# Kernel tuning notes

Measured on AMD Instinct MI355X. Metric: run time of the kernel, lower is better.

The kernel has to match this reference:

```python
import jax, jax.numpy as jnp
import numpy as np

B, S, H, DH = 2, 2048, 16, 64
DIM = H * DH          # 1024
WIN = 512             # relpos_win_size
LN_EPS = 1e-5


def setup_inputs() -> dict:
    key = jax.random.key(0)
    ks = jax.random.split(key, 8)
    return {
        "q": jax.random.normal(ks[0], (B, S, H, DH), dtype=jnp.float32),
        "k": jax.random.normal(ks[1], (B, S, H, DH), dtype=jnp.float32),
        "relpos_emb": jax.random.normal(ks[2], (WIN, DIM), dtype=jnp.float32),
        "ln_scale": jnp.ones((DIM,), dtype=jnp.float32),
        "ln_bias": jnp.zeros((DIM,), dtype=jnp.float32),
        "Wq": jax.random.normal(ks[3], (DIM, DIM), dtype=jnp.float32),
        "bq": jnp.zeros((DIM,), dtype=jnp.float32),
        "Wk": jax.random.normal(ks[4], (DIM, DIM), dtype=jnp.float32),
        "bk": jnp.zeros((DIM,), dtype=jnp.float32),
    }


def reference(q, k, relpos_emb, ln_scale, ln_bias, Wq, bq, Wk, bk):
    b, nq, h, dh = q.shape
    nk = k.shape[1]
    win = relpos_emb.shape[0]

    # LayerNorm over the embedding dim (use_pos_layer_norm=True); dropout is identity (eval).
    mu = jnp.mean(relpos_emb, axis=-1, keepdims=True)
    var = jnp.mean(jnp.square(relpos_emb - mu), axis=-1, keepdims=True)
    pe = (relpos_emb - mu) * jax.lax.rsqrt(var + LN_EPS) * ln_scale + ln_bias

    qpos = jnp.arange(nq)
    kpos = jnp.arange(nk)
    rel = jnp.clip(kpos[None, :] - qpos[:, None], -(win - 1), 0) + (win - 1)
    idx = jnp.broadcast_to(rel[None, None, :, :], (b, h, nq, nk))

    # Linear projections of the (small) relpos table, split into heads.
    relpos_k = (pe @ Wk.T + bk).reshape(win, h, dh)  # relpos_k_proj
    relpos_q = (pe @ Wq.T + bq).reshape(win, h, dh)  # relpos_q_proj

    # query-to-position: scores over window then gather along window axis (dim 3).
    query_pos_scores = jnp.einsum('bnhx,khx->bhnk', q, relpos_k)
    logits_query_pos = jnp.take_along_axis(query_pos_scores, idx, axis=3)  # [b,h,nq,nk]

    key_pos_scores = jnp.einsum('bnhx,khx->bhkn', k, relpos_q)
    logits_pos_key = jnp.take_along_axis(key_pos_scores, idx, axis=2)      # [b,h,nq,nk]

    # scale_factor = 1 + True + True = 3 (static constant, omitted from array outputs)
    return logits_pos_key, logits_query_pos, relpos_q, relpos_k
```

## Files before the change

### kernel.cpp

```cpp
#include <hip/hip_runtime.h>

#define BB 2
#define S 2048
#define H 16
#define DH 64
#define DIM 1024
#define WIN 512

#define OUT_PK 0
#define OUT_QP 134217728
#define OUT_RQ 268435456
#define OUT_RK 268959744

#define WS_C0Q   1024
#define WS_C511Q (1024 + 65536)
#define WS_C0K   (1024 + 2*65536)
#define WS_C511K (1024 + 3*65536)
#define WS_BF_BASE 263168

typedef short bf16x8 __attribute__((ext_vector_type(8)));
typedef float f32x4 __attribute__((ext_vector_type(4)));

__device__ inline short f2bf(float f) {
    union { float f; unsigned int u; } cv; cv.f = f;
    unsigned int u = cv.u + 0x7FFFu + ((cv.u >> 16) & 1u);
    return (short)(u >> 16);
}

__device__ inline float bf2f(short s) {
    union { unsigned int u; float f; } cv;
    cv.u = ((unsigned int)(unsigned short)s) << 16;
    return cv.f;
}

__global__ __launch_bounds__(256) void prep1(const float* __restrict__ emb,
        const float* __restrict__ lnsc, const float* __restrict__ lnbi,
        const float* __restrict__ Wq, const float* __restrict__ bq,
        const float* __restrict__ Wk, const float* __restrict__ bk,
        const float* __restrict__ q, const float* __restrict__ k,
        float* __restrict__ out, short* __restrict__ rqbf, short* __restrict__ rkbf,
        short* __restrict__ qbf, short* __restrict__ kbf) {
    __shared__ short As[64 * 72];
    __shared__ short Bs[64 * 72];
    __shared__ float smu[64];
    __shared__ float srs[64];
    int bid = blockIdx.x;
    int t = threadIdx.x;

    if (bid >= 256) {
        int cb = bid - 256;
        int z = cb >> 10;
        int blk = cb & 1023;
        const float* src = z ? k : q;
        short* dst = z ? kbf : qbf;
        int e0 = (blk * 256 + t) * 16;
        int c = e0 & 63, hh = (e0 >> 6) & 15, n = (e0 >> 10) & 2047, b = e0 >> 21;
        short* dbase = dst + (((size_t)(b * 16 + hh) * 2048) + n) * 64 + c;
#pragma unroll
        for (int i = 0; i < 4; ++i) {
            float4 v = *reinterpret_cast<const float4*>(src + e0 + i * 4);
            short4 o = { f2bf(v.x), f2bf(v.y), f2bf(v.z), f2bf(v.w) };
            *reinterpret_cast<short4*>(dbase + i * 4) = o;
        }
        return;
    }

    const float* W    = (bid >> 7) ? Wk : Wq;
    const float* bias = (bid >> 7) ? bk : bq;
    float* o = out + ((bid >> 7) ? OUT_RK : OUT_RQ);
    short* bfo = (bid >> 7) ? rkbf : rqbf;
    int r0 = (bid & 7) * 64;
    int d0 = ((bid >> 3) & 15) * 64;

    {
        int rr = t >> 2, p = t & 3;
        const float4* rp = reinterpret_cast<const float4*>(emb + (r0 + rr) * DIM + p * 256);
        float s = 0.f, sq = 0.f;
#pragma unroll
        for (int i = 0; i < 64; ++i) {
            float4 v = rp[i];
            s  += v.x + v.y + v.z + v.w;
            sq += v.x * v.x + v.y * v.y + v.z * v.z + v.w * v.w;
        }
        s += __shfl_xor(s, 1); sq += __shfl_xor(sq, 1);
        s += __shfl_xor(s, 2); sq += __shfl_xor(sq, 2);
        if (p == 0) {
            float mu = s / DIM;
            float var = sq / DIM - mu * mu;
            smu[rr] = mu;
            srs[rr] = rsqrtf(var + 1e-5f);
        }
    }
    __syncthreads();

    int lane = t & 63, w = t >> 6, lr = lane & 15, lg = lane >> 4;
    int srow = t >> 2, seg = (t & 3) * 16;
    float mu = smu[srow], rs = srs[srow];

    f32x4 acc[4] = {};
    for (int c0 = 0; c0 < DIM; c0 += 64) {
        const float4* ep = reinterpret_cast<const float4*>(emb + (size_t)(r0 + srow) * DIM + c0 + seg);
        const float4* wp = reinterpret_cast<const float4*>(W + (size_t)(d0 + srow) * DIM + c0 + seg);
        short4* ad = reinterpret_cast<short4*>(&As[srow * 72 + seg]);
        short4* wd = reinterpret_cast<short4*>(&Bs[srow * 72 + seg]);
#pragma unroll
        for (int i = 0; i < 4; ++i) {
            float4 v = ep[i], wv = wp[i];
            int cb2 = c0 + seg + i * 4;
            float4 sc = *reinterpret_cast<const float4*>(lnsc + cb2);
            float4 bi = *reinterpret_cast<const float4*>(lnbi + cb2);
            short4 a4 = { f2bf((v.x - mu) * rs * sc.x + bi.x),
                          f2bf((v.y - mu) * rs * sc.y + bi.y),
                          f2bf((v.z - mu) * rs * sc.z + bi.z),
                          f2bf((v.w - mu) * rs * sc.w + bi.w) };
            short4 w4 = { f2bf(wv.x), f2bf(wv.y), f2bf(wv.z), f2bf(wv.w) };
            ad[i] = a4;
            wd[i] = w4;
        }
        __syncthreads();
#pragma unroll
        for (int kk = 0; kk < 2; ++kk) {
            bf16x8 a = *reinterpret_cast<const bf16x8*>(&As[(w * 16 + lr) * 72 + kk * 32 + lg * 8]);
#pragma unroll
            for (int cg = 0; cg < 4; ++cg) {
                bf16x8 b = *reinterpret_cast<const bf16x8*>(&Bs[(cg * 16 + lr) * 72 + kk * 32 + lg * 8]);
                acc[cg] = __builtin_amdgcn_mfma_f32_16x16x32_bf16(a, b, acc[cg], 0, 0, 0);
            }
        }
        __syncthreads();
    }
#pragma unroll
    for (int cg = 0; cg < 4; ++cg) {
        int col = d0 + cg * 16 + lr;
        float bv = bias[col];
        int hh = col >> 6, cc = col & 63;
#pragma unroll
        for (int reg = 0; reg < 4; ++reg) {
            int rr = r0 + w * 16 + lg * 4 + reg;
            float val = acc[cg][reg] + bv;
            o[(size_t)rr * DIM + col] = val;
            bfo[((size_t)(hh * 512) + rr) * 64 + cc] = f2bf(val);
        }
    }
}

__global__ __launch_bounds__(256) void cvec(const short* __restrict__ qbf,
        const short* __restrict__ kbf, const short* __restrict__ rqbf,
        const short* __restrict__ rkbf, float* __restrict__ ws) {
    int cid = blockIdx.x;
    int z = cid >> 10;
    int rem = cid & 1023;
    int bh = rem >> 5, rb = rem & 31;
    int t = threadIdx.x;
    int rr = t >> 2, p = t & 3;
    int n = rb * 64 + rr;
    int h = bh & 15;
    const short* X = (z ? kbf : qbf) + ((size_t)bh * 2048 + n) * 64 + p * 16;
    const short* T = (z ? rqbf : rkbf) + (size_t)h * 512 * 64 + p * 16;
    bf16x8 x0 = *reinterpret_cast<const bf16x8*>(X);
    bf16x8 x1 = *reinterpret_cast<const bf16x8*>(X + 8);
    bf16x8 a0 = *reinterpret_cast<const bf16x8*>(T);
    bf16x8 a1 = *reinterpret_cast<const bf16x8*>(T + 8);
    bf16x8 c0 = *reinterpret_cast<const bf16x8*>(T + 511 * 64);
    bf16x8 c1 = *reinterpret_cast<const bf16x8*>(T + 511 * 64 + 8);
    float d0 = 0.f, d1 = 0.f;
#pragma unroll
    for (int e = 0; e < 8; ++e) {
        float xa = bf2f(x0[e]), xb = bf2f(x1[e]);
        d0 += xa * bf2f(a0[e]) + xb * bf2f(a1[e]);
        d1 += xa * bf2f(c0[e]) + xb * bf2f(c1[e]);
    }
    d0 += __shfl_xor(d0, 1); d0 += __shfl_xor(d0, 2);
    d1 += __shfl_xor(d1, 1); d1 += __shfl_xor(d1, 2);
    if (p == 0) {
        int o = bh * S + n;
        if (!z) { ws[WS_C0Q + o] = d0; ws[WS_C511Q + o] = d1; }
        else    { ws[WS_C0K + o] = d0; ws[WS_C511K + o] = d1; }
    }
}

__global__ __launch_bounds__(256) void outk(const short* __restrict__ qbf,
        const short* __restrict__ kbf, const short* __restrict__ rqbf,
        const short* __restrict__ rkbf, const float* __restrict__ ws,
        float* __restrict__ out) {
    __shared__ short Yt[64 * 132];

    int bid = blockIdx.x;
    int wg = (bid & 7) * 8192 + (bid >> 3);
    int PK = wg >> 15;
    int bh = (wg >> 10) & 31; int h = bh & 15;
    int nt = (wg >> 5) & 31, jt = wg & 31;
    int n0 = nt * 64, j0 = jt * 64;
    int jlo = nt > 8 ? nt - 8 : 0;
    int t = threadIdx.x;
    float* obase = out + (PK ? OUT_PK : OUT_QP) + (size_t)bh * S * S;

    if (jt < jlo || jt > nt) {
        int left = jt < jlo;
        const float* cv = ws + (PK ? (left ? WS_C0K : WS_C511K)
                                   : (left ? WS_C0Q : WS_C511Q)) + bh * S;
        int col4 = t & 15, r0w = t >> 4;
        if (PK) {
            f32x4 v = *reinterpret_cast<const f32x4*>(cv + j0 + col4 * 4);
#pragma unroll
            for (int i = 0; i < 4; ++i) {
                int n = n0 + r0w + i * 16;
                __builtin_nontemporal_store(v,
                    reinterpret_cast<f32x4*>(obase + (size_t)n * S + j0 + col4 * 4));
            }
        } else {
#pragma unroll
            for (int i = 0; i < 4; ++i) {
                int n = n0 + r0w + i * 16;
                float vs = cv[n];
                f32x4 v = { vs, vs, vs, vs };
                __builtin_nontemporal_store(v,
                    reinterpret_cast<f32x4*>(obase + (size_t)n * S + j0 + col4 * 4));
            }
        }
        return;
    }

    int rlo = 511 + j0 - (n0 + 63); rlo = rlo < 0 ? 0 : rlo;

    const short* xb = (PK ? kbf : qbf) + ((size_t)bh * 2048 + (PK ? j0 : n0)) * 64;
    const short* tbase = (PK ? rqbf : rkbf) + (size_t)h * 512 * 64;

    int lane = t & 63, w = t >> 6, lr = lane & 15, lg = lane >> 4;
    const short* arow = xb + (w * 16 + lr) * 64 + lg * 8;
    bf16x8 a0 = *reinterpret_cast<const bf16x8*>(arow);
    bf16x8 a1 = *reinterpret_cast<const bf16x8*>(arow + 32);

    bf16x8 b0s[8], b1s[8];
#pragma unroll
    for (int s = 0; s < 8; ++s) {
        int trow = rlo + s * 16 + lr;
        trow = trow > 511 ? 511 : trow;
        const short* brow = tbase + trow * 64 + lg * 8;
        b0s[s] = *reinterpret_cast<const bf16x8*>(brow);
        b1s[s] = *reinterpret_cast<const bf16x8*>(brow + 32);
    }
#pragma unroll
    for (int s = 0; s < 8; ++s) {
        f32x4 acc = {0.f, 0.f, 0.f, 0.f};
        acc = __builtin_amdgcn_mfma_f32_16x16x32_bf16(a0, b0s[s], acc, 0, 0, 0);
        acc = __builtin_amdgcn_mfma_f32_16x16x32_bf16(a1, b1s[s], acc, 0, 0, 0);
#pragma unroll
        for (int reg = 0; reg < 4; ++reg)
            Yt[(w * 16 + lg * 4 + reg) * 132 + s * 16 + lr] = f2bf(acc[reg]);
    }
    __syncthreads();

    int tx = t & 15, ty = t >> 4;
#pragma unroll
    for (int i = 0; i < 4; ++i) {
        int rowi = ty + i * 16;
        int n = n0 + rowi;
        float vv[4];
#pragma unroll
        for (int jj = 0; jj < 4; ++jj) {
            int j = j0 + tx * 4 + jj;
            int rel = 511 + j - n;
            rel = rel < 0 ? 0 : (rel > 511 ? 511 : rel);
            int g = rel - rlo;
            int m = PK ? (tx * 4 + jj) : rowi;
            vv[jj] = bf2f(Yt[m * 132 + g]);
        }
        f32x4 v = { vv[0], vv[1], vv[2], vv[3] };
        __builtin_nontemporal_store(v,
            reinterpret_cast<f32x4*>(obase + (size_t)n * S + j0 + tx * 4));
    }
}

extern "C" void kernel_launch(void* const* d_in, const int* in_sizes, int n_in,
                              void* d_out, int out_size, void* d_ws, size_t ws_size,
                              hipStream_t stream) {
    const float* q    = (const float*)d_in[0];
    const float* k    = (const float*)d_in[1];
    const float* emb  = (const float*)d_in[2];
    const float* lnsc = (const float*)d_in[3];
    const float* lnbi = (const float*)d_in[4];
    const float* Wq   = (const float*)d_in[5];
    const float* bq   = (const float*)d_in[6];
    const float* Wk   = (const float*)d_in[7];
    const float* bk   = (const float*)d_in[8];
    float* out = (float*)d_out;
    float* ws  = (float*)d_ws;

    short* qbf  = (short*)(ws + WS_BF_BASE);
    short* kbf  = qbf + (size_t)4194304;
    short* rqbf = kbf + (size_t)4194304;
    short* rkbf = rqbf + (size_t)524288;

    prep1<<<dim3(2304), dim3(256), 0, stream>>>(emb, lnsc, lnbi, Wq, bq, Wk, bk,
                                                q, k, out, rqbf, rkbf, qbf, kbf);
    cvec<<<dim3(2048), dim3(256), 0, stream>>>(qbf, kbf, rqbf, rkbf, ws);
    outk<<<dim3(65536), dim3(256), 0, stream>>>(qbf, kbf, rqbf, rkbf, ws, out);
}
```

Before: 233.4 us.

## Fuse clamp-vector computation into output kernel and merge flat tiles into wide panels

```diff
diff --git a/kernel.cpp b/kernel.cpp
--- a/kernel.cpp
+++ b/kernel.cpp
@@ -12,10 +12,6 @@
 #define OUT_RQ 268435456
 #define OUT_RK 268959744
 
-#define WS_C0Q   1024
-#define WS_C511Q (1024 + 65536)
-#define WS_C0K   (1024 + 2*65536)
-#define WS_C511K (1024 + 3*65536)
 #define WS_BF_BASE 263168
 
 typedef short bf16x8 __attribute__((ext_vector_type(8)));
@@ -31,6 +27,18 @@
     union { unsigned int u; float f; } cv;
     cv.u = ((unsigned int)(unsigned short)s) << 16;
     return cv.f;
+}
+
+__device__ inline float dot64(const short* __restrict__ x, const short* __restrict__ y) {
+    float d = 0.f;
+#pragma unroll
+    for (int c = 0; c < 8; ++c) {
+        bf16x8 a = *reinterpret_cast<const bf16x8*>(x + c * 8);
+        bf16x8 b = *reinterpret_cast<const bf16x8*>(y + c * 8);
+#pragma unroll
+        for (int e = 0; e < 8; ++e) d += bf2f(a[e]) * bf2f(b[e]);
+    }
+    return d;
 }
 
 __global__ __launch_bounds__(256) void prep1(const float* __restrict__ emb,
@@ -144,83 +152,92 @@
     }
 }
 
-__global__ __launch_bounds__(256) void cvec(const short* __restrict__ qbf,
-        const short* __restrict__ kbf, const short* __restrict__ rqbf,
-        const short* __restrict__ rkbf, float* __restrict__ ws) {
-    int cid = blockIdx.x;
-    int z = cid >> 10;
-    int rem = cid & 1023;
-    int bh = rem >> 5, rb = rem & 31;
-    int t = threadIdx.x;
-    int rr = t >> 2, p = t & 3;
-    int n = rb * 64 + rr;
-    int h = bh & 15;
-    const short* X = (z ? kbf : qbf) + ((size_t)bh * 2048 + n) * 64 + p * 16;
-    const short* T = (z ? rqbf : rkbf) + (size_t)h * 512 * 64 + p * 16;
-    bf16x8 x0 = *reinterpret_cast<const bf16x8*>(X);
-    bf16x8 x1 = *reinterpret_cast<const bf16x8*>(X + 8);
-    bf16x8 a0 = *reinterpret_cast<const bf16x8*>(T);
-    bf16x8 a1 = *reinterpret_cast<const bf16x8*>(T + 8);
-    bf16x8 c0 = *reinterpret_cast<const bf16x8*>(T + 511 * 64);
-    bf16x8 c1 = *reinterpret_cast<const bf16x8*>(T + 511 * 64 + 8);
-    float d0 = 0.f, d1 = 0.f;
-#pragma unroll
-    for (int e = 0; e < 8; ++e) {
-        float xa = bf2f(x0[e]), xb = bf2f(x1[e]);
-        d0 += xa * bf2f(a0[e]) + xb * bf2f(a1[e]);
-        d1 += xa * bf2f(c0[e]) + xb * bf2f(c1[e]);
-    }
-    d0 += __shfl_xor(d0, 1); d0 += __shfl_xor(d0, 2);
-    d1 += __shfl_xor(d1, 1); d1 += __shfl_xor(d1, 2);
-    if (p == 0) {
-        int o = bh * S + n;
-        if (!z) { ws[WS_C0Q + o] = d0; ws[WS_C511Q + o] = d1; }
-        else    { ws[WS_C0K + o] = d0; ws[WS_C511K + o] = d1; }
-    }
-}
-
 __global__ __launch_bounds__(256) void outk(const short* __restrict__ qbf,
         const short* __restrict__ kbf, const short* __restrict__ rqbf,
-        const short* __restrict__ rkbf, const float* __restrict__ ws,
-        float* __restrict__ out) {
+        const short* __restrict__ rkbf, float* __restrict__ out) {
     __shared__ short Yt[64 * 132];
+    float* c_sm = reinterpret_cast<float*>(Yt);
 
     int bid = blockIdx.x;
-    int wg = (bid & 7) * 8192 + (bid >> 3);
-    int PK = wg >> 15;
-    int bh = (wg >> 10) & 31; int h = bh & 15;
-    int nt = (wg >> 5) & 31, jt = wg & 31;
-    int n0 = nt * 64, j0 = jt * 64;
-    int jlo = nt > 8 ? nt - 8 : 0;
+    int wid = (bid & 7) * 3728 + (bid >> 3);
+    int panel = wid / 466, o = wid % 466;
+    int PK = panel >> 5, bh = panel & 31, h = bh & 15;
     int t = threadIdx.x;
     float* obase = out + (PK ? OUT_PK : OUT_QP) + (size_t)bh * S * S;
 
-    if (jt < jlo || jt > nt) {
-        int left = jt < jlo;
-        const float* cv = ws + (PK ? (left ? WS_C0K : WS_C511K)
-                                   : (left ? WS_C0Q : WS_C511Q)) + bh * S;
-        int col4 = t & 15, r0w = t >> 4;
+    int isflat, f = 0, bb = 0;
+    if (o < 428) { if (!(o & 1)) { isflat = 1; f = o >> 1; } else { isflat = 0; bb = o >> 1; } }
+    else         { isflat = 0; bb = 214 + (o - 428); }
+
+    if (isflat) {
+        int nt, j0, width, left;
+        if (f < 78) {
+            left = 1;
+            int rem = f;
+            nt = 9;
+            for (; nt <= 31; ++nt) { int c = (nt - 8 + 3) >> 2; if (rem < c) break; rem -= c; }
+            j0 = rem * 256;
+            width = (nt - 8) * 64 - j0; if (width > 256) width = 256;
+        } else {
+            left = 0;
+            int rem = f - 78;
+            nt = 0;
+            for (; nt <= 30; ++nt) { int c = (31 - nt + 3) >> 2; if (rem < c) break; rem -= c; }
+            j0 = (nt + 1) * 64 + rem * 256;
+            width = 2048 - j0; if (width > 256) width = 256;
+        }
+        int n0 = nt * 64;
+        int trow_off = left ? 0 : 511 * 64;
+
         if (PK) {
-            f32x4 v = *reinterpret_cast<const f32x4*>(cv + j0 + col4 * 4);
-#pragma unroll
-            for (int i = 0; i < 4; ++i) {
-                int n = n0 + r0w + i * 16;
-                __builtin_nontemporal_store(v,
-                    reinterpret_cast<f32x4*>(obase + (size_t)n * S + j0 + col4 * 4));
+            const short* trow = rqbf + (size_t)h * 512 * 64 + trow_off;
+            if (t < width) {
+                const short* xr = kbf + ((size_t)bh * 2048 + j0 + t) * 64;
+                c_sm[t] = dot64(xr, trow);
+            }
+            __syncthreads();
+            int w = t >> 6, lane = t & 63;
+            f32x4 cvv = {0.f, 0.f, 0.f, 0.f};
+            if (lane * 4 < width) cvv = *reinterpret_cast<const f32x4*>(&c_sm[lane * 4]);
+#pragma unroll
+            for (int i = 0; i < 16; ++i) {
+                int n = n0 + w * 16 + i;
+                if (lane * 4 < width)
+                    __builtin_nontemporal_store(cvv,
+                        reinterpret_cast<f32x4*>(obase + (size_t)n * S + j0 + lane * 4));
             }
         } else {
-#pragma unroll
-            for (int i = 0; i < 4; ++i) {
-                int n = n0 + r0w + i * 16;
-                float vs = cv[n];
+            const short* trow = rkbf + (size_t)h * 512 * 64 + trow_off;
+            if (t < 64) {
+                const short* xr = qbf + ((size_t)bh * 2048 + n0 + t) * 64;
+                c_sm[t] = dot64(xr, trow);
+            }
+            __syncthreads();
+            int w = t >> 6, lane = t & 63;
+#pragma unroll
+            for (int i = 0; i < 16; ++i) {
+                int row = w * 16 + i;
+                float vs = c_sm[row];
                 f32x4 v = { vs, vs, vs, vs };
-                __builtin_nontemporal_store(v,
-                    reinterpret_cast<f32x4*>(obase + (size_t)n * S + j0 + col4 * 4));
+                if (lane * 4 < width)
+                    __builtin_nontemporal_store(v,
+                        reinterpret_cast<f32x4*>(obase + (size_t)(n0 + row) * S + j0 + lane * 4));
             }
         }
         return;
     }
 
+    int r = bb, nt, jt;
+    if (r < 45) {
+        nt = 0;
+        while ((nt + 1) * (nt + 2) / 2 <= r) ++nt;
+        jt = r - nt * (nt + 1) / 2;
+    } else {
+        int r2 = r - 45;
+        nt = 9 + r2 / 9;
+        jt = nt - 8 + r2 % 9;
+    }
+    int n0 = nt * 64, j0 = jt * 64;
     int rlo = 511 + j0 - (n0 + 63); rlo = rlo < 0 ? 0 : rlo;
 
     const short* xb = (PK ? kbf : qbf) + ((size_t)bh * 2048 + (PK ? j0 : n0)) * 64;
@@ -294,6 +311,5 @@
 
     prep1<<<dim3(2304), dim3(256), 0, stream>>>(emb, lnsc, lnbi, Wq, bq, Wk, bk,
                                                 q, k, out, rqbf, rkbf, qbf, kbf);
-    cvec<<<dim3(2048), dim3(256), 0, stream>>>(qbf, kbf, rqbf, rkbf, ws);
-    outk<<<dim3(65536), dim3(256), 0, stream>>>(qbf, kbf, rqbf, rkbf, ws, out);
-}
+    outk<<<dim3(29824), dim3(256), 0, stream>>>(qbf, kbf, rqbf, rkbf, out);
+}
```

Result: slower. 284.9 us (+22.0%).
